# Optimization experiments

Measured on AMD Instinct MI355X. Metric: run time of the kernel, lower is better.

The kernel has to match this reference:

```python
import jax, jax.numpy as jnp
import numpy as np

B, S, HIDDEN = 2, 2048, 1024
NUM_HEADS, HEAD_DIM = 16, 64
STRIDE = 128
NEG = -10000.0


def _strided_mask(seq_len):
    # Sparse Transformer strided pattern: causal, local window of STRIDE,
    # plus every STRIDE-th previous position.
    i = jnp.arange(seq_len)[:, None]
    j = jnp.arange(seq_len)[None, :]
    diff = i - j
    allowed = (diff >= 0) & ((diff < STRIDE) | (diff % STRIDE == 0))
    return jnp.where(allowed, 0.0, NEG).astype(jnp.float32)  # [S, S]


def setup_inputs() -> dict:
    key = jax.random.key(0)
    k0, k1, k2, k3, k4 = jax.random.split(key, 5)
    hidden_states = jax.random.normal(k0, (B, S, HIDDEN), dtype=jnp.float32)
    attention_mask = jnp.zeros((B, 1, 1, S), dtype=jnp.float32)
    W_q = jax.random.normal(k1, (HIDDEN, HIDDEN), dtype=jnp.float32) * 0.02
    b_q = jnp.zeros((HIDDEN,), dtype=jnp.float32)
    W_v = jax.random.normal(k2, (HIDDEN, HIDDEN), dtype=jnp.float32) * 0.02
    b_v = jnp.zeros((HIDDEN,), dtype=jnp.float32)
    return {"hidden_states": hidden_states, "attention_mask": attention_mask,
            "W_q": W_q, "b_q": b_q, "W_v": W_v, "b_v": b_v}


def _heads(x):
    b, s, _ = x.shape
    return x.reshape(b, s, NUM_HEADS, HEAD_DIM).transpose(0, 2, 1, 3)  # [B,H,S,d]


def reference(hidden_states, attention_mask, W_q, b_q, W_v, b_v):
    q = _heads(hidden_states @ W_q + b_q)  # [B,H,S,d]
    v = _heads(hidden_states @ W_v + b_v)  # [B,H,S,d]
    hash_mask = _strided_mask(q.shape[-2])  # [S,S], broadcast over B,H
    # NB: source computes matmul(query, query^T) -- Q used for both sides.
    scores = jnp.einsum('bhid,bhjd->bhij', q, q) + hash_mask
    scores = scores / jnp.sqrt(jnp.asarray(HEAD_DIM, scores.dtype))
    scores = scores + attention_mask
    probs = jax.nn.softmax(scores, axis=-1)  # dropout p=0 (eval)
    ctx = jnp.einsum('bhij,bhjd->bhid', probs, v)  # [B,H,S,d]
    b = ctx.shape[0]
    return ctx.transpose(0, 2, 1, 3).reshape(b, -1, NUM_HEADS * HEAD_DIM)
```

## Files before the change

### kernel.cpp

```cpp
#include <hip/hip_runtime.h>

typedef __attribute__((ext_vector_type(8))) short short8;
typedef __attribute__((ext_vector_type(4))) float float4v;

__device__ inline float bf2f(ushort u) {
    unsigned v = ((unsigned)u) << 16;
    return __builtin_bit_cast(float, v);
}
__device__ inline ushort f2bf(float f) {
    unsigned u = __builtin_bit_cast(unsigned, f);
    u += 0x7FFFu + ((u >> 16) & 1u);
    return (ushort)(u >> 16);
}

__device__ inline void gload_lds16(const ushort* g, ushort* l) {
    __builtin_amdgcn_global_load_lds(
        (const __attribute__((address_space(1))) unsigned int*)g,
        (__attribute__((address_space(3))) unsigned int*)l,
        16, 0, 0);
}

__global__ __launch_bounds__(256) void prep(
    const float* __restrict__ hs, ushort* __restrict__ hsb,
    const float* __restrict__ Wq, const float* __restrict__ Wv,
    ushort* __restrict__ Wt) {
    __shared__ ushort tile[64][68];
    if (blockIdx.x < 1024) {
        const size_t base = ((size_t)blockIdx.x * 256 + threadIdx.x) * 16;
        union { ushort u[16]; uint4 v[2]; } o;
#pragma unroll
        for (int q = 0; q < 4; ++q) {
            float4v f = *(const float4v*)(hs + base + q * 4);
#pragma unroll
            for (int j = 0; j < 4; ++j) o.u[q * 4 + j] = f2bf(f[j]);
        }
        *(uint4*)(hsb + base)     = o.v[0];
        *(uint4*)(hsb + base + 8) = o.v[1];
        return;
    }
    const int idx = blockIdx.x - 1024;
    const int z = idx >> 8, yy = (idx >> 4) & 15, xx = idx & 15;
    const float* W = z ? Wv : Wq;
    ushort* Wto    = Wt + (z ? (size_t)1024 * 1024 : 0);
    const int k0 = yy * 64, n0 = xx * 64;
    const int tid = threadIdx.x;
    const int rr = tid >> 4;
    const int cc = (tid & 15) * 4;
    union U4 { ushort u[4]; uint2 v; };
#pragma unroll
    for (int i = 0; i < 4; ++i) {
        int row = rr + i * 16;
        float4v f = *(const float4v*)(W + (size_t)(k0 + row) * 1024 + n0 + cc);
        U4 x;
#pragma unroll
        for (int j = 0; j < 4; ++j) x.u[j] = f2bf(f[j]);
        *(uint2*)&tile[row][cc] = x.v;
    }
    __syncthreads();
#pragma unroll
    for (int i = 0; i < 4; ++i) {
        int row = rr + i * 16;
        U4 o;
#pragma unroll
        for (int j = 0; j < 4; ++j) o.u[j] = tile[cc + j][row];
        *(uint2*)(Wto + (size_t)(n0 + row) * 1024 + k0 + cc) = o.v;
    }
}

__global__ __launch_bounds__(512, 2) void qv_gemm(
    const ushort* __restrict__ hsb, const ushort* __restrict__ Wt,
    const float* __restrict__ bq, const float* __restrict__ bv,
    ushort* __restrict__ q_ws, ushort* __restrict__ v_ws) {
    __shared__ ushort smem[73728];
    const int m0 = blockIdx.y * 128, n0 = blockIdx.x * 256;
    const int tid  = threadIdx.x;
    const int wid  = tid >> 6, lane = tid & 63;
    const int quad = lane >> 4, l16 = lane & 15;
    const int wm = (wid >> 2) * 64;
    const int wn = (wid & 3) * 64;
    const int srow8 = tid >> 3;
    const int scb   = (tid & 7) * 16;

    auto stage = [&](int ktt, int bi, int r) {
        if (r < 2) {
            int row = r * 64 + srow8;
            int sb  = scb ^ ((row & 7) << 4);
            gload_lds16(hsb + (size_t)(m0 + row) * 1024 + ktt * 64 + (sb >> 1),
                        (ushort*)((char*)smem + bi * 49152 + r * 8192 + wid * 1024));
        } else {
            int row = (r - 2) * 64 + srow8;
            int sb  = scb ^ ((row & 7) << 4);
            gload_lds16(Wt + (size_t)(n0 + row) * 1024 + ktt * 64 + (sb >> 1),
                        (ushort*)((char*)smem + bi * 49152 + 16384 + (r - 2) * 8192 + wid * 1024));
        }
    };

    float4v acc[4][4] = {};

#pragma unroll
    for (int r = 0; r < 6; ++r) stage(0, 0, r);
#pragma unroll
    for (int r = 0; r < 6; ++r) stage(1, 1, r);

    int bi = 0;
    for (int ktt = 0; ktt < 16; ++ktt) {
        const char* Ab = (const char*)smem + bi * 49152;
        const char* Bb = Ab + 16384;

        if (ktt < 15) asm volatile("s_waitcnt vmcnt(6)" ::: "memory");
        else          asm volatile("s_waitcnt vmcnt(0)" ::: "memory");
        __builtin_amdgcn_s_barrier();
        __builtin_amdgcn_sched_barrier(0);

        short8 af[4][2], bfr[4][2];
#pragma unroll
        for (int mt = 0; mt < 4; ++mt) {
            int ar = wm + mt * 16 + l16;
            int sw = (ar & 7) << 4;
            af[mt][0] = *(const short8*)(Ab + ar * 128 + ((quad * 16) ^ sw));
        }
#pragma unroll
        for (int nt = 0; nt < 4; ++nt) {
            int br = wn + nt * 16 + l16;
            int sw = (br & 7) << 4;
            bfr[nt][0] = *(const short8*)(Bb + br * 128 + ((quad * 16) ^ sw));
        }
        __builtin_amdgcn_sched_barrier(0);
        const int kn = ktt + 2;
        const int b2 = (bi + 2 >= 3) ? bi - 1 : bi + 2;
        if (kn < 16) {
            stage(kn, b2, 0); stage(kn, b2, 1); stage(kn, b2, 2);
            stage(kn, b2, 3); stage(kn, b2, 4); stage(kn, b2, 5);
        }
#pragma unroll
        for (int mt = 0; mt < 4; ++mt) {
            int ar = wm + mt * 16 + l16;
            int sw = (ar & 7) << 4;
            af[mt][1] = *(const short8*)(Ab + ar * 128 + (((4 + quad) * 16) ^ sw));
        }
#pragma unroll
        for (int nt = 0; nt < 4; ++nt) {
            int br = wn + nt * 16 + l16;
            int sw = (br & 7) << 4;
            bfr[nt][1] = *(const short8*)(Bb + br * 128 + (((4 + quad) * 16) ^ sw));
        }
        __builtin_amdgcn_sched_barrier(0);
        asm volatile("s_waitcnt lgkmcnt(8)" ::: "memory");
        __builtin_amdgcn_sched_barrier(0);
        __builtin_amdgcn_s_setprio(1);
#pragma unroll
        for (int mt = 0; mt < 4; ++mt)
#pragma unroll
            for (int nt = 0; nt < 4; ++nt)
                acc[mt][nt] = __builtin_amdgcn_mfma_f32_16x16x32_bf16(
                    af[mt][0], bfr[nt][0], acc[mt][nt], 0, 0, 0);
        __builtin_amdgcn_s_setprio(0);
        asm volatile("s_waitcnt lgkmcnt(0)" ::: "memory");
        __builtin_amdgcn_sched_barrier(0);
        __builtin_amdgcn_s_setprio(1);
#pragma unroll
        for (int mt = 0; mt < 4; ++mt)
#pragma unroll
            for (int nt = 0; nt < 4; ++nt)
                acc[mt][nt] = __builtin_amdgcn_mfma_f32_16x16x32_bf16(
                    af[mt][1], bfr[nt][1], acc[mt][nt], 0, 0, 0);
        __builtin_amdgcn_s_setprio(0);

        bi = (bi + 1 >= 3) ? 0 : bi + 1;
    }

#pragma unroll
    for (int mt = 0; mt < 4; ++mt) {
#pragma unroll
        for (int nt = 0; nt < 4; ++nt) {
            int coln = n0 + wn + nt * 16 + l16;
            bool isq = coln < 1024;
            int c2 = isq ? coln : coln - 1024;
            float bsv = isq ? bq[c2] : bv[c2];
            ushort* outp = isq ? q_ws : v_ws;
            int hh = c2 >> 6, dd = c2 & 63;
#pragma unroll
            for (int reg = 0; reg < 4; ++reg) {
                int r = m0 + wm + mt * 16 + quad * 4 + reg;
                int bb = r >> 11, s = r & 2047;
                outp[(((size_t)bb * 16 + hh) * 2048 + s) * 64 + dd] =
                    f2bf(acc[mt][nt][reg] + bsv);
            }
        }
    }
}

__global__ __launch_bounds__(512, 4) void attn(
    const ushort* __restrict__ q_ws, const ushort* __restrict__ v_ws,
    const float* __restrict__ amask, float* __restrict__ out) {
    const int t = blockIdx.x, h = blockIdx.y, b = blockIdx.z;

    __shared__ ushort KwPl[16384];
    __shared__ ushort VtS[16384];
    __shared__ float  Sstr[128][17];
    __shared__ float  amw[256];

    const int tid = threadIdx.x;
    const int wid = tid >> 6, lane = tid & 63;
    const int quad = lane >> 4, l16 = lane & 15;
    const int r0 = wid * 16;
    const size_t qbase = ((size_t)b * 16 + h) * 2048 * 64;
    const int base_row = (t - 1) * 128;
    const int nk = (t >= 2) ? (t - 1) : 0;

    if (tid < 256) {
        int j = base_row + tid; if (j < 0) j = 0;
        amw[tid] = amask[(size_t)b * 2048 + j];
    }
#pragma unroll
    for (int i = 0; i < 4; ++i) {
        int u = tid + i * 512;
        int row = u >> 3, c = u & 7;
        int jg = base_row + row; if (jg < 0) jg = 0;
        *(uint4*)&KwPl[row * 64 + ((c ^ (row & 7)) * 8)] =
            *(const uint4*)(q_ws + qbase + (size_t)jg * 64 + c * 8);
    }
    {
        int j = tid & 255, dh0 = (tid >> 8) * 32;
        int jg = base_row + j; if (jg < 0) jg = 0;
        const ushort* src = v_ws + qbase + (size_t)jg * 64 + dh0;
        int cj = j >> 3, j7 = j & 7;
#pragma unroll
        for (int d = 0; d < 32; d += 8) {
            union { uint4 v; ushort u[8]; } tmp;
            tmp.v = *(const uint4*)(src + d);
#pragma unroll
            for (int jj = 0; jj < 8; ++jj) {
                int dd = dh0 + d + jj;
                VtS[dd * 256 + ((cj ^ (dd & 7)) * 8) + j7] = tmp.u[jj];
            }
        }
    }
    __syncthreads();

    float4v sacc[16] = {};
#pragma unroll
    for (int ks = 0; ks < 2; ++ks) {
        int c = ks * 4 + quad;
        int sw = (c ^ (l16 & 7)) * 8;
        short8 af = *(const short8*)&KwPl[(128 + r0 + l16) * 64 + sw];
#pragma unroll
        for (int nt = 0; nt < 16; ++nt) {
            short8 bfr = *(const short8*)&KwPl[(nt * 16 + l16) * 64 + sw];
            sacc[nt] = __builtin_amdgcn_mfma_f32_16x16x32_bf16(af, bfr, sacc[nt], 0, 0, 0);
        }
    }

    const int sr = tid >> 2;
    const int dq = (tid & 3) * 16;
    if (nk > 0) {
        float qv[16];
#pragma unroll
        for (int cc = 0; cc < 2; ++cc) {
            int c = (dq >> 3) + cc;
            union { uint4 v; ushort u[8]; } tm;
            tm.v = *(const uint4*)&KwPl[(128 + sr) * 64 + ((c ^ (sr & 7)) * 8)];
#pragma unroll
            for (int jj = 0; jj < 8; ++jj) qv[cc * 8 + jj] = bf2f(tm.u[jj]);
        }
        const size_t rbase = qbase + (size_t)sr * 64 + dq;
        uint4 ta = *(const uint4*)(q_ws + rbase);
        uint4 tb = *(const uint4*)(q_ws + rbase + 8);
        float amc = amask[(size_t)b * 2048 + sr];
        for (int k = 0; k < nk; ++k) {
            uint4 na = ta, nb = tb; float amn = amc;
            if (k + 1 < nk) {
                const ushort* kr = q_ws + rbase + ((size_t)(k + 1) << 13);
                na = *(const uint4*)kr; nb = *(const uint4*)(kr + 8);
                amn = amask[(size_t)b * 2048 + sr + ((k + 1) << 7)];
            }
            union { uint4 v; ushort u[8]; } t0, t1;
            t0.v = ta; t1.v = tb;
            float p = 0.f;
#pragma unroll
            for (int jj = 0; jj < 8; ++jj) p += qv[jj] * bf2f(t0.u[jj]);
#pragma unroll
            for (int jj = 0; jj < 8; ++jj) p += qv[8 + jj] * bf2f(t1.u[jj]);
            p += __shfl_xor(p, 1);
            p += __shfl_xor(p, 2);
            if ((tid & 3) == 0)
                Sstr[sr][k] = p * 0.125f + amc;
            ta = na; tb = nb; amc = amn;
        }
    }
    __syncthreads();

    unsigned pb[4][4];
#pragma unroll
    for (int reg = 0; reg < 4; ++reg) {
        int rr = r0 + quad * 4 + reg;
        float sv[16];
#pragma unroll
        for (int nt = 0; nt < 16; ++nt) {
            int c = nt * 16 + l16;
            bool allowed = (c >= rr) && (c <= rr + 128) && (t > 0 || c >= 128);
            sv[nt] = allowed ? sacc[nt][reg] * 0.125f + amw[c] : -INFINITY;
        }
        float sstr_v = (l16 < nk) ? Sstr[rr][l16] : -INFINITY;
        float m = sstr_v;
#pragma unroll
        for (int nt = 0; nt < 16; ++nt) m = fmaxf(m, sv[nt]);
#pragma unroll
        for (int off = 1; off < 16; off <<= 1) m = fmaxf(m, __shfl_xor(m, off));

        float es = (l16 < nk) ? __expf(sstr_v - m) : 0.f;
        float sum = es;
#pragma unroll
        for (int nt = 0; nt < 16; ++nt) {
            float e = (sv[nt] == -INFINITY) ? 0.f : __expf(sv[nt] - m);
            sv[nt] = e; sum += e;
        }
#pragma unroll
        for (int off = 1; off < 16; off <<= 1) sum += __shfl_xor(sum, off);
        float rden = 1.f / sum;
#pragma unroll
        for (int nt = 0; nt < 8; ++nt) {
            int c = nt * 2 + (l16 >> 3);
            KwPl[rr * 128 + ((c ^ (rr & 15)) * 8) + (l16 & 7)] = f2bf(sv[nt] * rden);
        }
#pragma unroll
        for (int i2 = 0; i2 < 4; ++i2) {
            unsigned lo = f2bf(sv[8 + 2 * i2] * rden);
            unsigned hi = f2bf(sv[9 + 2 * i2] * rden);
            pb[reg][i2] = lo | (hi << 16);
        }
        if (l16 < nk) Sstr[rr][l16] = es * rden;
    }
    __syncthreads();

    float4v cacc[4] = {};
#pragma unroll
    for (int ks = 0; ks < 4; ++ks) {
        int cp = ks * 4 + quad;
        short8 af = *(const short8*)&KwPl[(r0 + l16) * 128 + ((cp ^ l16) * 8)];
#pragma unroll
        for (int nt = 0; nt < 4; ++nt) {
            int sw = (cp ^ (l16 & 7)) * 8;
            short8 bfr = *(const short8*)&VtS[(nt * 16 + l16) * 256 + sw];
            cacc[nt] = __builtin_amdgcn_mfma_f32_16x16x32_bf16(af, bfr, cacc[nt], 0, 0, 0);
        }
    }
    __syncthreads();

#pragma unroll
    for (int reg = 0; reg < 4; ++reg) {
        int rr = r0 + quad * 4 + reg;
#pragma unroll
        for (int i2 = 0; i2 < 4; ++i2) {
            int nt0 = 8 + 2 * i2;
#pragma unroll
            for (int e2 = 0; e2 < 2; ++e2) {
                int nt = nt0 + e2;
                int c = (nt - 8) * 2 + (l16 >> 3);
                ushort val = (ushort)((pb[reg][i2] >> (16 * e2)) & 0xFFFF);
                KwPl[rr * 128 + ((c ^ (rr & 15)) * 8) + (l16 & 7)] = val;
            }
        }
    }
    __syncthreads();

#pragma unroll
    for (int ks = 0; ks < 4; ++ks) {
        int cp = ks * 4 + quad;
        short8 af = *(const short8*)&KwPl[(r0 + l16) * 128 + ((cp ^ l16) * 8)];
#pragma unroll
        for (int nt = 0; nt < 4; ++nt) {
            int cv = 16 + cp;
            int sw = (cv ^ (l16 & 7)) * 8;
            short8 bfr = *(const short8*)&VtS[(nt * 16 + l16) * 256 + sw];
            cacc[nt] = __builtin_amdgcn_mfma_f32_16x16x32_bf16(af, bfr, cacc[nt], 0, 0, 0);
        }
    }
    __syncthreads();

    float* ctxp = (float*)&VtS[0];
    {
        float acc16[16] = {};
        const size_t rbase = qbase + (size_t)sr * 64 + dq;
        if (nk > 0) {
            uint4 ta = *(const uint4*)(v_ws + rbase);
            uint4 tb = *(const uint4*)(v_ws + rbase + 8);
            for (int k = 0; k < nk; ++k) {
                uint4 na = ta, nb = tb;
                if (k + 1 < nk) {
                    const ushort* vr = v_ws + rbase + ((size_t)(k + 1) << 13);
                    na = *(const uint4*)vr; nb = *(const uint4*)(vr + 8);
                }
                float p = Sstr[sr][k];
                union { uint4 v; ushort u[8]; } t0, t1;
                t0.v = ta; t1.v = tb;
#pragma unroll
                for (int jj = 0; jj < 8; ++jj) acc16[jj] += p * bf2f(t0.u[jj]);
#pragma unroll
                for (int jj = 0; jj < 8; ++jj) acc16[8 + jj] += p * bf2f(t1.u[jj]);
                ta = na; tb = nb;
            }
        }
#pragma unroll
        for (int d4 = 0; d4 < 4; ++d4) {
            int c = (dq >> 2) + d4;
            *(float4v*)&ctxp[sr * 64 + ((c ^ (sr & 15)) * 4)] =
                *(const float4v*)&acc16[d4 * 4];
        }
    }
    __syncthreads();

    const size_t obase = ((size_t)b * 2048 + (size_t)t * 128) * 1024 + (size_t)h * 64;
#pragma unroll
    for (int nt = 0; nt < 4; ++nt)
#pragma unroll
        for (int reg = 0; reg < 4; ++reg) {
            int rr = r0 + quad * 4 + reg;
            int d = nt * 16 + l16;
            float cstr = ctxp[rr * 64 + (((d >> 2) ^ (rr & 15)) * 4) + (d & 3)];
            out[obase + (size_t)rr * 1024 + d] = cacc[nt][reg] + cstr;
        }
}

extern "C" void kernel_launch(void* const* d_in, const int* in_sizes, int n_in,
                              void* d_out, int out_size, void* d_ws, size_t ws_size,
                              hipStream_t stream) {
    int ihs = -1, iam = -1, iw1 = -1, iw2 = -1, ib1 = -1, ib2 = -1;
    for (int i = 0; i < n_in; ++i) {
        int s = in_sizes[i];
        if      (s == 4194304) { if (ihs < 0) ihs = i; }
        else if (s == 4096)    { if (iam < 0) iam = i; }
        else if (s == 1048576) { if (iw1 < 0) iw1 = i; else if (iw2 < 0) iw2 = i; }
        else if (s == 1024)    { if (ib1 < 0) ib1 = i; else if (ib2 < 0) ib2 = i; }
    }
    if (ihs < 0) ihs = 0; if (iam < 0) iam = 1;
    if (iw1 < 0) iw1 = 2; if (ib1 < 0) ib1 = 3;
    if (iw2 < 0) iw2 = 4; if (ib2 < 0) ib2 = 5;

    const float* hs    = (const float*)d_in[ihs];
    const float* amask = (const float*)d_in[iam];
    const float* Wq    = (const float*)d_in[iw1];
    const float* bq    = (const float*)d_in[ib1];
    const float* Wv    = (const float*)d_in[iw2];
    const float* bv    = (const float*)d_in[ib2];
    float* out = (float*)d_out;

    char* ws = (char*)d_ws;
    ushort* Wt   = (ushort*)(ws);
    ushort* hsb  = (ushort*)(ws + (1u << 22));
    ushort* q_ws = (ushort*)(ws + (1u << 22) + (1u << 23));
    ushort* v_ws = (ushort*)(ws + (1u << 22) + (2u << 23));

    prep<<<1536, 256, 0, stream>>>(hs, hsb, Wq, Wv, Wt);
    qv_gemm<<<dim3(8, 32), 512, 0, stream>>>(hsb, Wt, bq, bv, q_ws, v_ws);
    attn<<<dim3(16, 16, 2), 512, 0, stream>>>(q_ws, v_ws, amask, out);
}
```

Measured before the change: 134.2 us.

## Pipeline strided K/V loads, async LDS staging, and remap attention grid

The attention kernel now stages the K window into LDS with direct global-to-LDS loads. The V, mask and query-row loads are issued early, and the strided-key dot products and strided-value accumulation use a three-deep register prefetch ring in place of single-step double buffering. The V prefetch overlaps the PV MFMA phase, MFMA sections get raised wave priority, and the score buffer reuses the accumulator registers. Both kernels move to 1D grids, and attention blocks for the second batch run in reverse tile order to balance the triangular strided workload. The cost is more registers, hand-written waitcnt and barrier sequencing, and risk from the manual vmcnt accounting.

```diff
diff --git a/kernel.cpp b/kernel.cpp
--- a/kernel.cpp
+++ b/kernel.cpp
@@ -72,7 +72,9 @@
     const float* __restrict__ bq, const float* __restrict__ bv,
     ushort* __restrict__ q_ws, ushort* __restrict__ v_ws) {
     __shared__ ushort smem[73728];
-    const int m0 = blockIdx.y * 128, n0 = blockIdx.x * 256;
+    const int wg = blockIdx.x;
+    const int n0 = (wg & 7) * 256;
+    const int m0 = (wg >> 3) * 128;
     const int tid  = threadIdx.x;
     const int wid  = tid >> 6, lane = tid & 63;
     const int quad = lane >> 4, l16 = lane & 15;
@@ -190,10 +192,30 @@
     }
 }
 
+#define SISSUE(As, Bs, Ms, idx) { const ushort* kr_ = q_ws + srbase + ((size_t)(idx) << 13); \
+    As = *(const uint4*)kr_; Bs = *(const uint4*)(kr_ + 8); Ms = amask[amrow + ((idx) << 7)]; }
+#define SCONS(As, Bs, Ms, kk) { union { uint4 v; ushort u[8]; } t0_, t1_; t0_.v = As; t1_.v = Bs; \
+    float p_ = 0.f; \
+    _Pragma("unroll") for (int jj = 0; jj < 8; ++jj) p_ += qv[jj] * bf2f(t0_.u[jj]); \
+    _Pragma("unroll") for (int jj = 0; jj < 8; ++jj) p_ += qv[8 + jj] * bf2f(t1_.u[jj]); \
+    p_ += __shfl_xor(p_, 1); p_ += __shfl_xor(p_, 2); \
+    if ((tid & 3) == 0) Sstr[sr][kk] = p_ * 0.125f + Ms; }
+#define VISSUE(As, Bs, idx) { const ushort* vr_ = v_ws + srbase + ((size_t)(idx) << 13); \
+    As = *(const uint4*)vr_; Bs = *(const uint4*)(vr_ + 8); }
+#define VCONS(As, Bs, kk) { float p_ = Sstr[sr][kk]; union { uint4 v; ushort u[8]; } t0_, t1_; \
+    t0_.v = As; t1_.v = Bs; \
+    _Pragma("unroll") for (int jj = 0; jj < 8; ++jj) acc16[jj] += p_ * bf2f(t0_.u[jj]); \
+    _Pragma("unroll") for (int jj = 0; jj < 8; ++jj) acc16[8 + jj] += p_ * bf2f(t1_.u[jj]); }
+
 __global__ __launch_bounds__(512, 4) void attn(
     const ushort* __restrict__ q_ws, const ushort* __restrict__ v_ws,
     const float* __restrict__ amask, float* __restrict__ out) {
-    const int t = blockIdx.x, h = blockIdx.y, b = blockIdx.z;
+    const int wg = blockIdx.x;
+    const int half = wg >> 8, r5 = wg & 255;
+    const int t_raw = r5 & 15;
+    const int t = half ? (15 - t_raw) : t_raw;
+    const int h = r5 >> 4;
+    const int b = half;
 
     __shared__ ushort KwPl[16384];
     __shared__ ushort VtS[16384];
@@ -208,37 +230,65 @@
     const int base_row = (t - 1) * 128;
     const int nk = (t >= 2) ? (t - 1) : 0;
 
-    if (tid < 256) {
-        int j = base_row + tid; if (j < 0) j = 0;
-        amw[tid] = amask[(size_t)b * 2048 + j];
-    }
+    const int sr = tid >> 2;
+    const int dq = (tid & 3) * 16;
+    const size_t srbase = qbase + (size_t)sr * 64 + dq;
+    const size_t amrow  = (size_t)b * 2048 + sr;
+
 #pragma unroll
     for (int i = 0; i < 4; ++i) {
         int u = tid + i * 512;
         int row = u >> 3, c = u & 7;
         int jg = base_row + row; if (jg < 0) jg = 0;
-        *(uint4*)&KwPl[row * 64 + ((c ^ (row & 7)) * 8)] =
-            *(const uint4*)(q_ws + qbase + (size_t)jg * 64 + c * 8);
-    }
+        int sc = c ^ (row & 7);
+        gload_lds16(q_ws + qbase + (size_t)jg * 64 + sc * 8, &KwPl[u * 8]);
+    }
+    __builtin_amdgcn_sched_barrier(0);
+
+    const int vj = tid & 255, dh0 = (tid >> 8) * 32;
+    int vjg = base_row + vj; if (vjg < 0) vjg = 0;
+    const ushort* vsrc = v_ws + qbase + (size_t)vjg * 64 + dh0;
+    uint4 vt0 = *(const uint4*)(vsrc);
+    uint4 vt1 = *(const uint4*)(vsrc + 8);
+    uint4 vt2 = *(const uint4*)(vsrc + 16);
+    uint4 vt3 = *(const uint4*)(vsrc + 24);
+    int amj = base_row + (tid & 255); if (amj < 0) amj = 0;
+    float amv = amask[(size_t)b * 2048 + amj];
+    uint4 qr0 = *(const uint4*)(q_ws + qbase + (size_t)(t * 128 + sr) * 64 + dq);
+    uint4 qr1 = *(const uint4*)(q_ws + qbase + (size_t)(t * 128 + sr) * 64 + dq + 8);
+
+    uint4 kA0{}, kB0{}, kA1{}, kB1{}, kA2{}, kB2{};
+    float am0 = 0.f, am1 = 0.f, am2 = 0.f;
+    if (nk > 0) {
+        SISSUE(kA0, kB0, am0, 0);
+        SISSUE(kA1, kB1, am1, (1 < nk ? 1 : 0));
+        SISSUE(kA2, kB2, am2, (2 < nk ? 2 : 0));
+    }
+
     {
-        int j = tid & 255, dh0 = (tid >> 8) * 32;
-        int jg = base_row + j; if (jg < 0) jg = 0;
-        const ushort* src = v_ws + qbase + (size_t)jg * 64 + dh0;
-        int cj = j >> 3, j7 = j & 7;
-#pragma unroll
-        for (int d = 0; d < 32; d += 8) {
-            union { uint4 v; ushort u[8]; } tmp;
-            tmp.v = *(const uint4*)(src + d);
-#pragma unroll
-            for (int jj = 0; jj < 8; ++jj) {
-                int dd = dh0 + d + jj;
-                VtS[dd * 256 + ((cj ^ (dd & 7)) * 8) + j7] = tmp.u[jj];
-            }
-        }
-    }
-    __syncthreads();
+        int cj = vj >> 3, j7 = vj & 7;
+        union { uint4 v; ushort u[8]; } tmp;
+        tmp.v = vt0;
+#pragma unroll
+        for (int jj = 0; jj < 8; ++jj) { int dd = dh0 + jj;      VtS[dd * 256 + (((cj) ^ (dd & 7)) * 8) + j7] = tmp.u[jj]; }
+        tmp.v = vt1;
+#pragma unroll
+        for (int jj = 0; jj < 8; ++jj) { int dd = dh0 + 8 + jj;  VtS[dd * 256 + (((cj) ^ (dd & 7)) * 8) + j7] = tmp.u[jj]; }
+        tmp.v = vt2;
+#pragma unroll
+        for (int jj = 0; jj < 8; ++jj) { int dd = dh0 + 16 + jj; VtS[dd * 256 + (((cj) ^ (dd & 7)) * 8) + j7] = tmp.u[jj]; }
+        tmp.v = vt3;
+#pragma unroll
+        for (int jj = 0; jj < 8; ++jj) { int dd = dh0 + 24 + jj; VtS[dd * 256 + (((cj) ^ (dd & 7)) * 8) + j7] = tmp.u[jj]; }
+    }
+    amw[tid & 255] = amv;
+
+    asm volatile("s_waitcnt vmcnt(8) lgkmcnt(0)" ::: "memory");
+    __builtin_amdgcn_s_barrier();
+    __builtin_amdgcn_sched_barrier(0);
 
     float4v sacc[16] = {};
+    __builtin_amdgcn_s_setprio(1);
 #pragma unroll
     for (int ks = 0; ks < 2; ++ks) {
         int c = ks * 4 + quad;
@@ -250,42 +300,25 @@
             sacc[nt] = __builtin_amdgcn_mfma_f32_16x16x32_bf16(af, bfr, sacc[nt], 0, 0, 0);
         }
     }
-
-    const int sr = tid >> 2;
-    const int dq = (tid & 3) * 16;
+    __builtin_amdgcn_s_setprio(0);
+
     if (nk > 0) {
         float qv[16];
-#pragma unroll
-        for (int cc = 0; cc < 2; ++cc) {
-            int c = (dq >> 3) + cc;
-            union { uint4 v; ushort u[8]; } tm;
-            tm.v = *(const uint4*)&KwPl[(128 + sr) * 64 + ((c ^ (sr & 7)) * 8)];
-#pragma unroll
-            for (int jj = 0; jj < 8; ++jj) qv[cc * 8 + jj] = bf2f(tm.u[jj]);
-        }
-        const size_t rbase = qbase + (size_t)sr * 64 + dq;
-        uint4 ta = *(const uint4*)(q_ws + rbase);
-        uint4 tb = *(const uint4*)(q_ws + rbase + 8);
-        float amc = amask[(size_t)b * 2048 + sr];
-        for (int k = 0; k < nk; ++k) {
-            uint4 na = ta, nb = tb; float amn = amc;
+        union { uint4 v; ushort u[8]; } qa, qb;
+        qa.v = qr0; qb.v = qr1;
+#pragma unroll
+        for (int jj = 0; jj < 8; ++jj) { qv[jj] = bf2f(qa.u[jj]); qv[8 + jj] = bf2f(qb.u[jj]); }
+        for (int k = 0; k < nk; k += 3) {
+            SCONS(kA0, kB0, am0, k);
+            if (k + 3 < nk) SISSUE(kA0, kB0, am0, k + 3);
             if (k + 1 < nk) {
-                const ushort* kr = q_ws + rbase + ((size_t)(k + 1) << 13);
-                na = *(const uint4*)kr; nb = *(const uint4*)(kr + 8);
-                amn = amask[(size_t)b * 2048 + sr + ((k + 1) << 7)];
-            }
-            union { uint4 v; ushort u[8]; } t0, t1;
-            t0.v = ta; t1.v = tb;
-            float p = 0.f;
-#pragma unroll
-            for (int jj = 0; jj < 8; ++jj) p += qv[jj] * bf2f(t0.u[jj]);
-#pragma unroll
-            for (int jj = 0; jj < 8; ++jj) p += qv[8 + jj] * bf2f(t1.u[jj]);
-            p += __shfl_xor(p, 1);
-            p += __shfl_xor(p, 2);
-            if ((tid & 3) == 0)
-                Sstr[sr][k] = p * 0.125f + amc;
-            ta = na; tb = nb; amc = amn;
+                SCONS(kA1, kB1, am1, k + 1);
+                if (k + 4 < nk) SISSUE(kA1, kB1, am1, k + 4);
+            }
+            if (k + 2 < nk) {
+                SCONS(kA2, kB2, am2, k + 2);
+                if (k + 5 < nk) SISSUE(kA2, kB2, am2, k + 5);
+            }
         }
     }
     __syncthreads();
@@ -294,17 +327,16 @@
 #pragma unroll
     for (int reg = 0; reg < 4; ++reg) {
         int rr = r0 + quad * 4 + reg;
-        float sv[16];
+        float sstr_v = (l16 < nk) ? Sstr[rr][l16] : -INFINITY;
+        float m = sstr_v;
 #pragma unroll
         for (int nt = 0; nt < 16; ++nt) {
             int c = nt * 16 + l16;
             bool allowed = (c >= rr) && (c <= rr + 128) && (t > 0 || c >= 128);
-            sv[nt] = allowed ? sacc[nt][reg] * 0.125f + amw[c] : -INFINITY;
-        }
-        float sstr_v = (l16 < nk) ? Sstr[rr][l16] : -INFINITY;
-        float m = sstr_v;
-#pragma unroll
-        for (int nt = 0; nt < 16; ++nt) m = fmaxf(m, sv[nt]);
+            float x = allowed ? sacc[nt][reg] * 0.125f + amw[c] : -INFINITY;
+            sacc[nt][reg] = x;
+            m = fmaxf(m, x);
+        }
 #pragma unroll
         for (int off = 1; off < 16; off <<= 1) m = fmaxf(m, __shfl_xor(m, off));
 
@@ -312,8 +344,9 @@
         float sum = es;
 #pragma unroll
         for (int nt = 0; nt < 16; ++nt) {
-            float e = (sv[nt] == -INFINITY) ? 0.f : __expf(sv[nt] - m);
-            sv[nt] = e; sum += e;
+            float x = sacc[nt][reg];
+            float e = (x == -INFINITY) ? 0.f : __expf(x - m);
+            sacc[nt][reg] = e; sum += e;
         }
 #pragma unroll
         for (int off = 1; off < 16; off <<= 1) sum += __shfl_xor(sum, off);
@@ -321,19 +354,27 @@
 #pragma unroll
         for (int nt = 0; nt < 8; ++nt) {
             int c = nt * 2 + (l16 >> 3);
-            KwPl[rr * 128 + ((c ^ (rr & 15)) * 8) + (l16 & 7)] = f2bf(sv[nt] * rden);
+            KwPl[rr * 128 + ((c ^ (rr & 15)) * 8) + (l16 & 7)] = f2bf(sacc[nt][reg] * rden);
         }
 #pragma unroll
         for (int i2 = 0; i2 < 4; ++i2) {
-            unsigned lo = f2bf(sv[8 + 2 * i2] * rden);
-            unsigned hi = f2bf(sv[9 + 2 * i2] * rden);
+            unsigned lo = f2bf(sacc[8 + 2 * i2][reg] * rden);
+            unsigned hi = f2bf(sacc[9 + 2 * i2][reg] * rden);
             pb[reg][i2] = lo | (hi << 16);
         }
         if (l16 < nk) Sstr[rr][l16] = es * rden;
     }
     __syncthreads();
 
+    uint4 vA0{}, vB0{}, vA1{}, vB1{}, vA2{}, vB2{};
+    if (nk > 0) {
+        VISSUE(vA0, vB0, 0);
+        VISSUE(vA1, vB1, (1 < nk ? 1 : 0));
+        VISSUE(vA2, vB2, (2 < nk ? 2 : 0));
+    }
+
     float4v cacc[4] = {};
+    __builtin_amdgcn_s_setprio(1);
 #pragma unroll
     for (int ks = 0; ks < 4; ++ks) {
         int cp = ks * 4 + quad;
@@ -345,6 +386,7 @@
             cacc[nt] = __builtin_amdgcn_mfma_f32_16x16x32_bf16(af, bfr, cacc[nt], 0, 0, 0);
         }
     }
+    __builtin_amdgcn_s_setprio(0);
     __syncthreads();
 
 #pragma unroll
@@ -364,6 +406,7 @@
     }
     __syncthreads();
 
+    __builtin_amdgcn_s_setprio(1);
 #pragma unroll
     for (int ks = 0; ks < 4; ++ks) {
         int cp = ks * 4 + quad;
@@ -376,37 +419,31 @@
             cacc[nt] = __builtin_amdgcn_mfma_f32_16x16x32_bf16(af, bfr, cacc[nt], 0, 0, 0);
         }
     }
+    __builtin_amdgcn_s_setprio(0);
+
+    float acc16[16] = {};
+    if (nk > 0) {
+        for (int k = 0; k < nk; k += 3) {
+            VCONS(vA0, vB0, k);
+            if (k + 3 < nk) VISSUE(vA0, vB0, k + 3);
+            if (k + 1 < nk) {
+                VCONS(vA1, vB1, k + 1);
+                if (k + 4 < nk) VISSUE(vA1, vB1, k + 4);
+            }
+            if (k + 2 < nk) {
+                VCONS(vA2, vB2, k + 2);
+                if (k + 5 < nk) VISSUE(vA2, vB2, k + 5);
+            }
+        }
+    }
     __syncthreads();
 
     float* ctxp = (float*)&VtS[0];
-    {
-        float acc16[16] = {};
-        const size_t rbase = qbase + (size_t)sr * 64 + dq;
-        if (nk > 0) {
-            uint4 ta = *(const uint4*)(v_ws + rbase);
-            uint4 tb = *(const uint4*)(v_ws + rbase + 8);
-            for (int k = 0; k < nk; ++k) {
-                uint4 na = ta, nb = tb;
-                if (k + 1 < nk) {
-                    const ushort* vr = v_ws + rbase + ((size_t)(k + 1) << 13);
-                    na = *(const uint4*)vr; nb = *(const uint4*)(vr + 8);
-                }
-                float p = Sstr[sr][k];
-                union { uint4 v; ushort u[8]; } t0, t1;
-                t0.v = ta; t1.v = tb;
-#pragma unroll
-                for (int jj = 0; jj < 8; ++jj) acc16[jj] += p * bf2f(t0.u[jj]);
-#pragma unroll
-                for (int jj = 0; jj < 8; ++jj) acc16[8 + jj] += p * bf2f(t1.u[jj]);
-                ta = na; tb = nb;
-            }
-        }
-#pragma unroll
-        for (int d4 = 0; d4 < 4; ++d4) {
-            int c = (dq >> 2) + d4;
-            *(float4v*)&ctxp[sr * 64 + ((c ^ (sr & 15)) * 4)] =
-                *(const float4v*)&acc16[d4 * 4];
-        }
+#pragma unroll
+    for (int d4 = 0; d4 < 4; ++d4) {
+        int c = (dq >> 2) + d4;
+        *(float4v*)&ctxp[sr * 64 + ((c ^ (sr & 15)) * 4)] =
+            *(const float4v*)&acc16[d4 * 4];
     }
     __syncthreads();
 
@@ -452,6 +489,6 @@
     ushort* v_ws = (ushort*)(ws + (1u << 22) + (2u << 23));
 
     prep<<<1536, 256, 0, stream>>>(hs, hsb, Wq, Wv, Wt);
-    qv_gemm<<<dim3(8, 32), 512, 0, stream>>>(hsb, Wt, bq, bv, q_ws, v_ws);
-    attn<<<dim3(16, 16, 2), 512, 0, stream>>>(q_ws, v_ws, amask, out);
-}
+    qv_gemm<<<256, 512, 0, stream>>>(hsb, Wt, bq, bv, q_ws, v_ws);
+    attn<<<512, 512, 0, stream>>>(q_ws, v_ws, amask, out);
+}
```

Measured after the change: 141.2 us. 1.05x slower.
